# Kernel tuning notes

Hardware: AMD Instinct MI355X
Metric: run time of the kernel (lower is better)

## Reference

```python
import jax, jax.numpy as jnp
import numpy as np

B, D_IN, H, K = 16384, 256, 1024, 16


def setup_inputs() -> dict:
    key = jax.random.key(0)
    k_x, k_idx, k_w1, k_w2 = jax.random.split(key, 4)
    x = jax.random.normal(k_x, (B, D_IN), dtype=jnp.float32)
    input_indices = jax.random.randint(k_idx, (H, K), 0, D_IN, dtype=jnp.int64)
    w1 = jax.random.normal(k_w1, (H, K), dtype=jnp.float32) * np.sqrt(2.0 / K).astype(np.float32)
    b1 = jnp.zeros((H,), dtype=jnp.float32)
    w2 = jax.random.normal(k_w2, (1, H), dtype=jnp.float32) * np.sqrt(2.0 / H).astype(np.float32)
    b2 = jnp.zeros((1,), dtype=jnp.float32)
    return {"x": x, "input_indices": input_indices, "w1": w1, "b1": b1, "w2": w2, "b2": b2}


def reference(x, input_indices, w1, b1, w2, b2):
    # Gather per-neuron inputs: [B, H, K] (vectorized form of the torch per-h loop)
    selected = x[:, input_indices]
    # Per-neuron weighted sum + bias, tanh
    pre_act = jnp.einsum('bhk,hk->bh', selected, w1) + b1  # [B, H]
    hidden = jnp.tanh(pre_act)
    # Output linear + tanh, squeeze to [B]
    out = jnp.tanh(hidden @ w2.T + b2)  # [B, 1]
    return out.squeeze(-1)
```

## Files before the change

kernel.cpp:

```cpp
#include <hip/hip_runtime.h>
#include <hip/hip_fp16.h>

#define NB 16384
#define ND 256
#define NH 1024
#define NK 16

using f16x8 = __attribute__((ext_vector_type(8))) _Float16;
using f32x4 = __attribute__((ext_vector_type(4))) float;

__device__ __forceinline__ float fast_tanh(float x) {
    float e = __expf(2.0f * x);
    return 1.0f - 2.0f * __builtin_amdgcn_rcpf(e + 1.0f);
}

__global__ __launch_bounds__(256) void build_w_kernel(
        const int* __restrict__ idx, const float* __restrict__ w1,
        _Float16* __restrict__ Wf) {
    int t = blockIdx.x * 256 + threadIdx.x;
    int h = t >> 5;
    int g = t & 31;
    int d0 = g << 3;
    float a[8];
#pragma unroll
    for (int e = 0; e < 8; ++e) a[e] = 0.f;
#pragma unroll
    for (int k = 0; k < NK; ++k) {
        int iv = idx[h * NK + k];
        float wv = w1[h * NK + k];
#pragma unroll
        for (int e = 0; e < 8; ++e)
            if (iv == d0 + e) a[e] += wv;
    }
    int c  = h >> 4;
    int ml = h & 15;
    int ks = g >> 2;
    int kg = g & 3;
    size_t off = (((size_t)(c * 8 + ks)) * 64 + kg * 16 + ml) * 8;
    f16x8 o;
#pragma unroll
    for (int e = 0; e < 8; ++e) o[e] = (_Float16)a[e];
    *reinterpret_cast<f16x8*>(&Wf[off]) = o;
}

__global__ __launch_bounds__(512, 2) void fused_kernel(
        const float* __restrict__ x, const _Float16* __restrict__ Wf,
        const float* __restrict__ b1, const float* __restrict__ w2,
        const float* __restrict__ b2, float* __restrict__ out) {
    __shared__ _Float16 lA[64 * 256];
    __shared__ float red[8 * 64];

    const int t = threadIdx.x;
    const int lane = t & 63;
    const int w = t >> 6;
    const int gm0 = blockIdx.x * 64;
    const int ml = lane & 15;
    const int kg = lane >> 4;

    const int sr  = t >> 3;
    const int sub = t & 7;
    const float4* xsrc = reinterpret_cast<const float4*>(
        x + (size_t)(gm0 + sr) * ND + sub * 32);
    float4 v[8];
#pragma unroll
    for (int j = 0; j < 8; ++j) v[j] = xsrc[j];

    const _Float16* gB = Wf + (size_t)w * 32768 + (size_t)lane * 8;
    f16x8 bA[4], bB[4];
#pragma unroll
    for (int ks = 0; ks < 4; ++ks)
        bA[ks] = *reinterpret_cast<const f16x8*>(gB + ks * 512);
#pragma unroll
    for (int ks = 0; ks < 4; ++ks)
        bB[ks] = *reinterpret_cast<const f16x8*>(gB + 2048 + ks * 512);

#pragma unroll
    for (int q = 0; q < 4; ++q) {
        int c = sub * 4 + q;
        f16x8 hh;
        hh[0] = (_Float16)v[2*q].x;   hh[1] = (_Float16)v[2*q].y;
        hh[2] = (_Float16)v[2*q].z;   hh[3] = (_Float16)v[2*q].w;
        hh[4] = (_Float16)v[2*q+1].x; hh[5] = (_Float16)v[2*q+1].y;
        hh[6] = (_Float16)v[2*q+1].z; hh[7] = (_Float16)v[2*q+1].w;
        int a16 = sr * 32 + (c ^ (sr & 7));
        *reinterpret_cast<f16x8*>(&lA[a16 * 8]) = hh;
    }
    __syncthreads();

    f16x8 af[4][8];
#pragma unroll
    for (int mi = 0; mi < 4; ++mi)
#pragma unroll
        for (int ks = 0; ks < 8; ++ks) {
            int r = mi * 16 + ml;
            int c = ks * 4 + kg;
            af[mi][ks] = *reinterpret_cast<const f16x8*>(
                &lA[(r * 32 + (c ^ (r & 7))) * 8]);
        }

    float rowpart[4][4];
#pragma unroll
    for (int mi = 0; mi < 4; ++mi)
#pragma unroll
        for (int r4 = 0; r4 < 4; ++r4) rowpart[mi][r4] = 0.f;

    const _Float16* pb0 = gB + 4096;
    const _Float16* pb1 = gB + 4096 + 2048;
    const float* b1p = b1 + w * 128 + ml;
    const float* w2p = w2 + w * 128 + ml;

#pragma unroll 1
    for (int nc = 0; nc < 8; ++nc) {
        f32x4 acc[4];
#pragma unroll
        for (int mi = 0; mi < 4; ++mi) acc[mi] = f32x4{0.f, 0.f, 0.f, 0.f};

#pragma unroll
        for (int ks = 0; ks < 4; ++ks)
#pragma unroll
            for (int mi = 0; mi < 4; ++mi)
                acc[mi] = __builtin_amdgcn_mfma_f32_16x16x32_f16(
                    af[mi][ks], bA[ks], acc[mi], 0, 0, 0);
        if (nc != 7) {
#pragma unroll
            for (int ks = 0; ks < 4; ++ks)
                bA[ks] = *reinterpret_cast<const f16x8*>(pb0 + ks * 512);
        }

#pragma unroll
        for (int ks = 0; ks < 4; ++ks)
#pragma unroll
            for (int mi = 0; mi < 4; ++mi)
                acc[mi] = __builtin_amdgcn_mfma_f32_16x16x32_f16(
                    af[mi][4 + ks], bB[ks], acc[mi], 0, 0, 0);
        if (nc != 7) {
#pragma unroll
            for (int ks = 0; ks < 4; ++ks)
                bB[ks] = *reinterpret_cast<const f16x8*>(pb1 + ks * 512);
        }
        pb0 += 4096;
        pb1 += 4096;

        float b1v = b1p[nc * 16];
        float w2v = w2p[nc * 16];
#pragma unroll
        for (int mi = 0; mi < 4; ++mi)
#pragma unroll
            for (int r4 = 0; r4 < 4; ++r4)
                rowpart[mi][r4] += fast_tanh(acc[mi][r4] + b1v) * w2v;
    }

#pragma unroll
    for (int mi = 0; mi < 4; ++mi)
#pragma unroll
        for (int r4 = 0; r4 < 4; ++r4) {
            float vv = rowpart[mi][r4];
            vv += __shfl_xor(vv, 1);
            vv += __shfl_xor(vv, 2);
            vv += __shfl_xor(vv, 4);
            vv += __shfl_xor(vv, 8);
            rowpart[mi][r4] = vv;
        }
    if (ml == 0) {
#pragma unroll
        for (int mi = 0; mi < 4; ++mi)
#pragma unroll
            for (int r4 = 0; r4 < 4; ++r4)
                red[w * 64 + mi * 16 + kg * 4 + r4] = rowpart[mi][r4];
    }
    __syncthreads();

    if (t < 64) {
        float s = 0.f;
#pragma unroll
        for (int j = 0; j < 8; ++j) s += red[j * 64 + t];
        out[gm0 + t] = fast_tanh(s + b2[0]);
    }
}

extern "C" void kernel_launch(void* const* d_in, const int* in_sizes, int n_in,
                              void* d_out, int out_size, void* d_ws, size_t ws_size,
                              hipStream_t stream) {
    const float* x   = (const float*)d_in[0];
    const int*   idx = (const int*)d_in[1];
    const float* w1  = (const float*)d_in[2];
    const float* b1  = (const float*)d_in[3];
    const float* w2  = (const float*)d_in[4];
    const float* b2  = (const float*)d_in[5];
    float* out = (float*)d_out;

    _Float16* Wf = (_Float16*)d_ws;

    build_w_kernel<<<(NH * 32) / 256, 256, 0, stream>>>(idx, w1, Wf);
    fused_kernel<<<NB / 64, 512, 0, stream>>>(x, Wf, b1, w2, b2, out);
}
```

Measured before the change: 22.34 us.

## Stagger weight chunk order per block/wave, vectorize build loads, add MFMA priority

Each wave now starts its loop over the eight N-chunks at an offset derived from the block index and wave id. This is meant to spread concurrent reads of the shared weight buffer across different addresses and cache channels instead of having every block hit the same chunk at once. The b1/w2 loads move to the top of each iteration and are indexed by the rotated chunk. s_setprio raises wave priority around the MFMA bursts. The weight-build kernel now reads indices and weights as int4/float4 vectors and launches 128-thread blocks.

```diff
diff --git a/kernel.cpp b/kernel.cpp
--- a/kernel.cpp
+++ b/kernel.cpp
@@ -14,23 +14,32 @@
     return 1.0f - 2.0f * __builtin_amdgcn_rcpf(e + 1.0f);
 }
 
-__global__ __launch_bounds__(256) void build_w_kernel(
+__device__ __forceinline__ void scat8(float (&a)[8], int ii, float ww, int d0) {
+#pragma unroll
+    for (int e = 0; e < 8; ++e)
+        if (ii == d0 + e) a[e] += ww;
+}
+
+__global__ __launch_bounds__(128) void build_w_kernel(
         const int* __restrict__ idx, const float* __restrict__ w1,
         _Float16* __restrict__ Wf) {
-    int t = blockIdx.x * 256 + threadIdx.x;
+    int t = blockIdx.x * 128 + threadIdx.x;
     int h = t >> 5;
     int g = t & 31;
     int d0 = g << 3;
+    const int4*   ip = reinterpret_cast<const int4*>(idx + h * NK);
+    const float4* wp = reinterpret_cast<const float4*>(w1 + h * NK);
     float a[8];
 #pragma unroll
     for (int e = 0; e < 8; ++e) a[e] = 0.f;
 #pragma unroll
-    for (int k = 0; k < NK; ++k) {
-        int iv = idx[h * NK + k];
-        float wv = w1[h * NK + k];
-#pragma unroll
-        for (int e = 0; e < 8; ++e)
-            if (iv == d0 + e) a[e] += wv;
+    for (int j = 0; j < 4; ++j) {
+        int4   I = ip[j];
+        float4 V = wp[j];
+        scat8(a, I.x, V.x, d0);
+        scat8(a, I.y, V.y, d0);
+        scat8(a, I.z, V.z, d0);
+        scat8(a, I.w, V.w, d0);
     }
     int c  = h >> 4;
     int ml = h & 15;
@@ -56,6 +65,7 @@
     const int gm0 = blockIdx.x * 64;
     const int ml = lane & 15;
     const int kg = lane >> 4;
+    const int start = ((blockIdx.x >> 3) + w) & 7;
 
     const int sr  = t >> 3;
     const int sub = t & 7;
@@ -65,14 +75,17 @@
 #pragma unroll
     for (int j = 0; j < 8; ++j) v[j] = xsrc[j];
 
-    const _Float16* gB = Wf + (size_t)w * 32768 + (size_t)lane * 8;
+    const _Float16* gW = Wf + (size_t)w * 32768 + (size_t)lane * 8;
     f16x8 bA[4], bB[4];
-#pragma unroll
-    for (int ks = 0; ks < 4; ++ks)
-        bA[ks] = *reinterpret_cast<const f16x8*>(gB + ks * 512);
-#pragma unroll
-    for (int ks = 0; ks < 4; ++ks)
-        bB[ks] = *reinterpret_cast<const f16x8*>(gB + 2048 + ks * 512);
+    {
+        const _Float16* p0 = gW + start * 4096;
+#pragma unroll
+        for (int ks = 0; ks < 4; ++ks)
+            bA[ks] = *reinterpret_cast<const f16x8*>(p0 + ks * 512);
+#pragma unroll
+        for (int ks = 0; ks < 4; ++ks)
+            bB[ks] = *reinterpret_cast<const f16x8*>(p0 + 2048 + ks * 512);
+    }
 
 #pragma unroll
     for (int q = 0; q < 4; ++q) {
@@ -104,45 +117,47 @@
 #pragma unroll
         for (int r4 = 0; r4 < 4; ++r4) rowpart[mi][r4] = 0.f;
 
-    const _Float16* pb0 = gB + 4096;
-    const _Float16* pb1 = gB + 4096 + 2048;
-    const float* b1p = b1 + w * 128 + ml;
-    const float* w2p = w2 + w * 128 + ml;
-
 #pragma unroll 1
     for (int nc = 0; nc < 8; ++nc) {
+        const int ncc = (start + nc) & 7;
+        float b1v = b1[w * 128 + ncc * 16 + ml];
+        float w2v = w2[w * 128 + ncc * 16 + ml];
+
         f32x4 acc[4];
 #pragma unroll
         for (int mi = 0; mi < 4; ++mi) acc[mi] = f32x4{0.f, 0.f, 0.f, 0.f};
 
+        const int ncn = (start + nc + 1) & 7;
+        const _Float16* pn = gW + ncn * 4096;
+
+        __builtin_amdgcn_s_setprio(1);
 #pragma unroll
         for (int ks = 0; ks < 4; ++ks)
 #pragma unroll
             for (int mi = 0; mi < 4; ++mi)
                 acc[mi] = __builtin_amdgcn_mfma_f32_16x16x32_f16(
                     af[mi][ks], bA[ks], acc[mi], 0, 0, 0);
+        __builtin_amdgcn_s_setprio(0);
         if (nc != 7) {
 #pragma unroll
             for (int ks = 0; ks < 4; ++ks)
-                bA[ks] = *reinterpret_cast<const f16x8*>(pb0 + ks * 512);
-        }
-
+                bA[ks] = *reinterpret_cast<const f16x8*>(pn + ks * 512);
+        }
+
+        __builtin_amdgcn_s_setprio(1);
 #pragma unroll
         for (int ks = 0; ks < 4; ++ks)
 #pragma unroll
             for (int mi = 0; mi < 4; ++mi)
                 acc[mi] = __builtin_amdgcn_mfma_f32_16x16x32_f16(
                     af[mi][4 + ks], bB[ks], acc[mi], 0, 0, 0);
+        __builtin_amdgcn_s_setprio(0);
         if (nc != 7) {
 #pragma unroll
             for (int ks = 0; ks < 4; ++ks)
-                bB[ks] = *reinterpret_cast<const f16x8*>(pb1 + ks * 512);
-        }
-        pb0 += 4096;
-        pb1 += 4096;
-
-        float b1v = b1p[nc * 16];
-        float w2v = w2p[nc * 16];
+                bB[ks] = *reinterpret_cast<const f16x8*>(pn + 2048 + ks * 512);
+        }
+
 #pragma unroll
         for (int mi = 0; mi < 4; ++mi)
 #pragma unroll
@@ -191,6 +206,6 @@
 
     _Float16* Wf = (_Float16*)d_ws;
 
-    build_w_kernel<<<(NH * 32) / 256, 256, 0, stream>>>(idx, w1, Wf);
+    build_w_kernel<<<(NH * 32) / 128, 128, 0, stream>>>(idx, w1, Wf);
     fused_kernel<<<NB / 64, 512, 0, stream>>>(x, Wf, b1, w2, b2, out);
 }
```

Result: no change. 22.46 us (+0.5%).
